# Optimization experiments

Measured on AMD Instinct MI355X. Metric: run time of the kernel, lower is better.

Reference implementation:

```python
import jax, jax.numpy as jnp
import numpy as np

B, N, D, H, KD, VD, O = 64, 2048, 256, 8, 32, 32, 256
LARGE = 1e9
EPS = 1e-10


def setup_inputs() -> dict:
    key = jax.random.key(0)
    ks = jax.random.split(key, 8)
    return {
        "q_data": jax.random.normal(ks[0], (B, N, D), dtype=jnp.float32),
        "m_data": jax.random.normal(ks[1], (B, N, D), dtype=jnp.float32),
        "q_mask": jnp.ones((B, N, 1), dtype=jnp.float32),
        "query_w": jax.random.normal(ks[2], (D, H, KD), dtype=jnp.float32) * 0.05,
        "key_w": jax.random.normal(ks[3], (D, KD), dtype=jnp.float32) * 0.05,
        "value_w": jax.random.normal(ks[4], (D, VD), dtype=jnp.float32) * 0.05,
        "gating_w": jax.random.normal(ks[5], (D, H, VD), dtype=jnp.float32) * 0.05,
        "gating_b": jnp.ones((H, VD), dtype=jnp.float32),
        "output_w": jax.random.normal(ks[6], (H, VD, O), dtype=jnp.float32) * 0.05,
        "output_b": jnp.zeros((O,), dtype=jnp.float32),
    }


def reference(q_data, m_data, q_mask, query_w, key_w, value_w, gating_w, gating_b, output_w, output_b):
    key_dim = query_w.shape[-1]
    # values/keys are shared across heads: [B, N, KD/VD]
    v = jnp.einsum('bka,ac->bkc', m_data, value_w)
    # masked mean over the query axis -> single query per batch element
    q_avg = jnp.sum(q_mask * q_data, axis=1) / (jnp.sum(q_mask, axis=1) + EPS)  # [B, D]
    q = jnp.einsum('ba,ahc->bhc', q_avg, query_w) * (key_dim ** -0.5)  # [B, H, KD]
    k = jnp.einsum('bka,ac->bkc', m_data, key_w)  # [B, N, KD]
    bias = LARGE * (q_mask[:, None, :, 0] - 1.0)  # [B, 1, N]
    logits = jnp.einsum('bhc,bkc->bhk', q, k) + bias  # [B, H, N]
    weights = jax.nn.softmax(logits, axis=-1)
    weighted_avg = jnp.einsum('bhk,bkc->bhc', weights, v)  # [B, H, VD]
    gate = jax.nn.sigmoid(jnp.einsum('bqc,chv->bqhv', q_data, gating_w) + gating_b)  # [B, N, H, VD]
    gated = weighted_avg[:, None] * gate  # broadcast single attn result over queries
    return jnp.einsum('bqhc,hco->bqo', gated, output_w) + output_b  # [B, N, O]
```

## Files before the change

kernel.cpp:

```cpp
#include <hip/hip_runtime.h>

#define B_ 64
#define N_ 2048
#define D_ 256
#define H_ 8
#define LARGE_ 1e9f
#define EPS_ 1e-10f

typedef __attribute__((ext_vector_type(4))) float f32x4;
typedef __attribute__((ext_vector_type(8))) short s16x8;

#define WS_QSUM 0
#define WS_MSUM 65536
#define WS_ZERO 65792
#define WS_QKBF 66048
#define WS_LOG  590336
#define WS_WMP  4784640
#define WS_WGP  6881792
#define WS_WPP  7012864

__device__ __forceinline__ unsigned short f2bf(float f) {
  union { float f; unsigned u; } v; v.f = f;
  unsigned r = v.u + 0x7fffu + ((v.u >> 16) & 1u);
  return (unsigned short)(r >> 16);
}
__device__ __forceinline__ float bf2f(unsigned short s) {
  union { unsigned u; float f; } v; v.u = ((unsigned)s) << 16;
  return v.f;
}

__global__ void kA(const float* __restrict__ q_data, const float* __restrict__ q_mask,
                   const float* __restrict__ gating_w, float* __restrict__ q_sum,
                   float* __restrict__ mask_sum, unsigned short* __restrict__ wgp) {
  int blk = blockIdx.x, t = threadIdx.x;
  if (blk < 512) {
    int b = blk >> 3, n0 = (blk & 7) * 256;
    __shared__ float msk[256];
    __shared__ float mred[4];
    msk[t] = q_mask[b * N_ + n0 + t];
    __syncthreads();
    int w = t >> 6, d4 = t & 63;
    const float* qbase = q_data + ((size_t)(b * N_ + n0)) * D_;
    f32x4 acc = {0.f, 0.f, 0.f, 0.f};
    #pragma unroll 4
    for (int i = 0; i < 64; ++i) {
      int r = i * 4 + w;
      f32x4 v = *(const f32x4*)(qbase + (size_t)r * D_ + d4 * 4);
      float mk = msk[r];
      acc += v * mk;
    }
    float* qs = q_sum + b * D_ + d4 * 4;
    atomicAdd(qs + 0, acc[0]);
    atomicAdd(qs + 1, acc[1]);
    atomicAdd(qs + 2, acc[2]);
    atomicAdd(qs + 3, acc[3]);
    float mv = msk[t];
    for (int off = 32; off; off >>= 1) mv += __shfl_xor(mv, off);
    if ((t & 63) == 0) mred[t >> 6] = mv;
    __syncthreads();
    if (t == 0) atomicAdd(&mask_sum[b], mred[0] + mred[1] + mred[2] + mred[3]);
  } else {
    int base = (blk - 512) * 1024;
    for (int i = 0; i < 4; ++i) {
      int a = base + i * 256 + t;
      int sc = a >> 9, l = (a >> 3) & 63, j = a & 7;
      int s = sc >> 4, c = sc & 15, lh = l >> 4, ll = l & 15;
      int k = s * 32 + lh * 8 + j, n = c * 16 + ll;
      wgp[a] = f2bf(gating_w[k * 256 + n]);
    }
  }
}

__global__ void kB(const float* __restrict__ q_sum, const float* __restrict__ mask_sum,
                   const float* __restrict__ query_w, const float* __restrict__ key_w,
                   unsigned short* __restrict__ qkbf) {
  int b = blockIdx.x, t = threadIdx.x;
  __shared__ float qa[256];
  __shared__ float ql[256];
  float inv = 1.f / (mask_sum[b] + EPS_);
  qa[t] = q_sum[b * 256 + t] * inv;
  __syncthreads();
  float s = 0.f;
  #pragma unroll 4
  for (int a = 0; a < 256; ++a) s += qa[a] * query_w[a * 256 + t];
  ql[t] = s * 0.17677669529663687f;
  __syncthreads();
  float v8[8];
  #pragma unroll
  for (int h = 0; h < 8; ++h) {
    float v = 0.f;
    #pragma unroll
    for (int c = 0; c < 32; ++c) v += key_w[t * 32 + c] * ql[h * 32 + c];
    v8[h] = v;
  }
  int si = t >> 5, lh = (t >> 3) & 3, j = t & 7;
  unsigned short* base = qkbf + ((size_t)(b * 8 + si) * 64) * 8;
  #pragma unroll
  for (int h = 0; h < 8; ++h) {
    base[(lh * 16 + h) * 8 + j] = f2bf(v8[h]);
    base[(lh * 16 + 8 + h) * 8 + j] = 0;
  }
}

__global__ void kC(const float* __restrict__ m_data, const float* __restrict__ q_mask,
                   const unsigned short* __restrict__ qkbf, float* __restrict__ logits) {
  int b = blockIdx.y, n0 = blockIdx.x * 64, t = threadIdx.x;
  __shared__ __align__(16) unsigned char sM[64 * 528];
  {
    int w = t >> 6, d4 = t & 63;
    #pragma unroll
    for (int i = 0; i < 16; ++i) {
      int r = i * 4 + w;
      f32x4 v = *(const f32x4*)(m_data + ((size_t)(b * N_ + n0 + r)) * D_ + d4 * 4);
      uint2 pp;
      pp.x = f2bf(v[0]) | ((unsigned)f2bf(v[1]) << 16);
      pp.y = f2bf(v[2]) | ((unsigned)f2bf(v[3]) << 16);
      *(uint2*)(sM + r * 528 + d4 * 8) = pp;
    }
  }
  __syncthreads();
  int lane = t & 63, w = t >> 6;
  int l15 = lane & 15, lhi = lane >> 4;
  const s16x8* A = (const s16x8*)qkbf + (size_t)b * 512;
  s16x8 areg[8];
  #pragma unroll
  for (int s = 0; s < 8; ++s) areg[s] = A[s * 64 + lane];
  f32x4 acc = {0.f, 0.f, 0.f, 0.f};
  int nrow = w * 16 + l15;
  #pragma unroll
  for (int s = 0; s < 8; ++s) {
    s16x8 bfr = *(const s16x8*)(sM + nrow * 528 + s * 64 + lhi * 16);
    acc = __builtin_amdgcn_mfma_f32_16x16x32_bf16(areg[s], bfr, acc, 0, 0, 0);
  }
  if (lhi < 2) {
    int n = n0 + nrow;
    float bias = LARGE_ * (q_mask[b * N_ + n] - 1.f);
    f32x4 st = acc + bias;
    *(f32x4*)(logits + ((size_t)(b * N_ + n)) * 8 + lhi * 4) = st;
  }
}

__global__ void kS(float* __restrict__ wbuf) {
  int b = blockIdx.x, t = threadIdx.x;
  int lane = t & 63, w = t >> 6;
  __shared__ float sred[4][8];
  __shared__ float Mh[8];
  __shared__ float Sh[8];
  f32x4 lv[16];
  f32x4* base = (f32x4*)(wbuf + (size_t)b * N_ * 8) + t * 16;
  #pragma unroll
  for (int i = 0; i < 16; ++i) lv[i] = base[i];
  float pm[8];
  #pragma unroll
  for (int h = 0; h < 8; ++h) pm[h] = -3.4e38f;
  #pragma unroll
  for (int k = 0; k < 8; ++k)
    #pragma unroll
    for (int hh = 0; hh < 2; ++hh)
      #pragma unroll
      for (int c = 0; c < 4; ++c)
        pm[hh * 4 + c] = fmaxf(pm[hh * 4 + c], lv[k * 2 + hh][c]);
  for (int off = 32; off; off >>= 1)
    #pragma unroll
    for (int h = 0; h < 8; ++h) pm[h] = fmaxf(pm[h], __shfl_xor(pm[h], off));
  if (lane == 0)
    #pragma unroll
    for (int h = 0; h < 8; ++h) sred[w][h] = pm[h];
  __syncthreads();
  if (t < 8) Mh[t] = fmaxf(fmaxf(sred[0][t], sred[1][t]), fmaxf(sred[2][t], sred[3][t]));
  __syncthreads();
  float M[8], ps[8];
  #pragma unroll
  for (int h = 0; h < 8; ++h) { M[h] = Mh[h]; ps[h] = 0.f; }
  #pragma unroll
  for (int k = 0; k < 8; ++k)
    #pragma unroll
    for (int hh = 0; hh < 2; ++hh)
      #pragma unroll
      for (int c = 0; c < 4; ++c) {
        float e = __expf(lv[k * 2 + hh][c] - M[hh * 4 + c]);
        lv[k * 2 + hh][c] = e;
        ps[hh * 4 + c] += e;
      }
  for (int off = 32; off; off >>= 1)
    #pragma unroll
    for (int h = 0; h < 8; ++h) ps[h] += __shfl_xor(ps[h], off);
  if (lane == 0)
    #pragma unroll
    for (int h = 0; h < 8; ++h) sred[w][h] = ps[h];
  __syncthreads();
  if (t < 8) Sh[t] = sred[0][t] + sred[1][t] + sred[2][t] + sred[3][t];
  __syncthreads();
  float rs[8];
  #pragma unroll
  for (int h = 0; h < 8; ++h) rs[h] = 1.f / Sh[h];
  #pragma unroll
  for (int k = 0; k < 8; ++k)
    #pragma unroll
    for (int hh = 0; hh < 2; ++hh)
      #pragma unroll
      for (int c = 0; c < 4; ++c) lv[k * 2 + hh][c] *= rs[hh * 4 + c];
  #pragma unroll
  for (int i = 0; i < 16; ++i) base[i] = lv[i];
}

__global__ void kE(const float* __restrict__ m_data, const float* __restrict__ wbuf,
                   unsigned short* __restrict__ wm_part) {
  int b = blockIdx.y, n0 = blockIdx.x * 256, t = threadIdx.x;
  __shared__ float wb[2048];
  __shared__ float red[4 * 8 * 256];
  {
    const f32x4* src = (const f32x4*)(wbuf + ((size_t)b * N_ + n0) * 8);
    f32x4* dst = (f32x4*)wb;
    dst[t] = src[t];
    dst[t + 256] = src[t + 256];
  }
  __syncthreads();
  int w = t >> 6, l = t & 63;
  f32x4 acc[8];
  #pragma unroll
  for (int h = 0; h < 8; ++h) acc[h] = (f32x4){0.f, 0.f, 0.f, 0.f};
  const float* mbase = m_data + ((size_t)(b * N_ + n0 + w * 64)) * D_ + l * 4;
  #pragma unroll 2
  for (int i = 0; i < 64; ++i) {
    f32x4 mv = *(const f32x4*)(mbase + (size_t)i * D_);
    const f32x4* wrow = (const f32x4*)(wb + (w * 64 + i) * 8);
    f32x4 w0 = wrow[0], w1 = wrow[1];
    acc[0] += mv * w0[0]; acc[1] += mv * w0[1]; acc[2] += mv * w0[2]; acc[3] += mv * w0[3];
    acc[4] += mv * w1[0]; acc[5] += mv * w1[1]; acc[6] += mv * w1[2]; acc[7] += mv * w1[3];
  }
  #pragma unroll
  for (int h = 0; h < 8; ++h) *(f32x4*)(&red[(w * 8 + h) * 256 + l * 4]) = acc[h];
  __syncthreads();
  float s8[8];
  #pragma unroll
  for (int h = 0; h < 8; ++h)
    s8[h] = red[h * 256 + t] + red[(8 + h) * 256 + t] + red[(16 + h) * 256 + t] +
            red[(24 + h) * 256 + t];
  uint4 u;
  u.x = f2bf(s8[0]) | ((unsigned)f2bf(s8[1]) << 16);
  u.y = f2bf(s8[2]) | ((unsigned)f2bf(s8[3]) << 16);
  u.z = f2bf(s8[4]) | ((unsigned)f2bf(s8[5]) << 16);
  u.w = f2bf(s8[6]) | ((unsigned)f2bf(s8[7]) << 16);
  *(uint4*)(wm_part + ((size_t)((b * 8 + blockIdx.x) * 256 + t)) * 8) = u;
}

__global__ void kF(const unsigned short* __restrict__ wm_part, const float* __restrict__ value_w,
                   const float* __restrict__ output_w, unsigned short* __restrict__ wpp) {
  int blk = blockIdx.x, t = threadIdx.x;
  int b = blk >> 2, quad = blk & 3;
  __shared__ float wml[8 * 256];
  __shared__ float wa[256];
  {
    float s8[8] = {0.f, 0.f, 0.f, 0.f, 0.f, 0.f, 0.f, 0.f};
    #pragma unroll
    for (int p = 0; p < 8; ++p) {
      uint4 u = *(const uint4*)(wm_part + ((size_t)((b * 8 + p) * 256 + t)) * 8);
      s8[0] += bf2f(u.x & 0xffff); s8[1] += bf2f(u.x >> 16);
      s8[2] += bf2f(u.y & 0xffff); s8[3] += bf2f(u.y >> 16);
      s8[4] += bf2f(u.z & 0xffff); s8[5] += bf2f(u.z >> 16);
      s8[6] += bf2f(u.w & 0xffff); s8[7] += bf2f(u.w >> 16);
    }
    #pragma unroll
    for (int h = 0; h < 8; ++h) wml[h * 256 + t] = s8[h];
  }
  __syncthreads();
  {
    int h = t >> 5, v = t & 31;
    float s = 0.f;
    #pragma unroll 4
    for (int d = 0; d < 256; ++d) s += wml[h * 256 + d] * value_w[d * 32 + v];
    wa[t] = s;
  }
  __syncthreads();
  unsigned short* wp = wpp + (size_t)b * 65536;
  int base = quad * 16384;
  for (int it = 0; it < 64; ++it) {
    int a = base + it * 256 + t;
    int sc = a >> 9, l = (a >> 3) & 63, j = a & 7;
    int s = sc >> 4, c = sc & 15, lh = l >> 4, ll = l & 15;
    int hv = s * 32 + lh * 8 + j, o = c * 16 + ll;
    wp[a] = f2bf(wa[hv] * output_w[hv * 256 + o]);
  }
}

__global__ void __launch_bounds__(256, 4) kG(
    const float* __restrict__ q_data, const float* __restrict__ gating_b,
    const float* __restrict__ output_b, const unsigned short* __restrict__ wgp,
    const unsigned short* __restrict__ wpp, float* __restrict__ out) {
  int b = blockIdx.y, row0 = blockIdx.x * 64, t = threadIdx.x;
  __shared__ __align__(16) unsigned char sG[64 * 528];
  {
    int w = t >> 6, d4 = t & 63;
    #pragma unroll
    for (int i = 0; i < 16; ++i) {
      int r = i * 4 + w;
      f32x4 v = *(const f32x4*)(q_data + ((size_t)(b * N_ + row0 + r)) * D_ + d4 * 4);
      uint2 pp;
      pp.x = f2bf(v[0]) | ((unsigned)f2bf(v[1]) << 16);
      pp.y = f2bf(v[2]) | ((unsigned)f2bf(v[3]) << 16);
      *(uint2*)(sG + r * 528 + d4 * 8) = pp;
    }
  }
  __syncthreads();
  int lane = t & 63, cg = t >> 6;
  int l15 = lane & 15, lhi = lane >> 4;
  const f32x4 z = {0.f, 0.f, 0.f, 0.f};
  f32x4 acc[16];
  #pragma unroll
  for (int f = 0; f < 16; ++f) acc[f] = z;
  const s16x8* Bg = (const s16x8*)wgp;
  #pragma unroll
  for (int s = 0; s < 8; ++s) {
    s16x8 af[4], bfr[4];
    #pragma unroll
    for (int rt = 0; rt < 4; ++rt)
      af[rt] = *(const s16x8*)(sG + (rt * 16 + l15) * 528 + s * 64 + lhi * 16);
    #pragma unroll
    for (int ct = 0; ct < 4; ++ct) bfr[ct] = Bg[(s * 16 + cg * 4 + ct) * 64 + lane];
    #pragma unroll
    for (int rt = 0; rt < 4; ++rt)
      #pragma unroll
      for (int ct = 0; ct < 4; ++ct)
        acc[rt * 4 + ct] =
            __builtin_amdgcn_mfma_f32_16x16x32_bf16(af[rt], bfr[ct], acc[rt * 4 + ct], 0, 0, 0);
  }
  __syncthreads();
  {
    float gb[4];
    #pragma unroll
    for (int ct = 0; ct < 4; ++ct) gb[ct] = gating_b[cg * 64 + ct * 16 + l15];
    #pragma unroll
    for (int rt = 0; rt < 4; ++rt)
      #pragma unroll
      for (int ct = 0; ct < 4; ++ct) {
        int col = cg * 64 + ct * 16 + l15;
        #pragma unroll
        for (int r = 0; r < 4; ++r) {
          float x = acc[rt * 4 + ct][r] + gb[ct];
          float g = 1.f / (1.f + __expf(-x));
          int row = rt * 16 + lhi * 4 + r;
          *(unsigned short*)(sG + row * 528 + col * 2) = f2bf(g);
        }
      }
  }
  __syncthreads();
  #pragma unroll
  for (int f = 0; f < 16; ++f) acc[f] = z;
  const s16x8* Bp = (const s16x8*)wpp + (size_t)b * 8192;
  #pragma unroll
  for (int s = 0; s < 8; ++s) {
    s16x8 af[4], bfr[4];
    #pragma unroll
    for (int rt = 0; rt < 4; ++rt)
      af[rt] = *(const s16x8*)(sG + (rt * 16 + l15) * 528 + s * 64 + lhi * 16);
    #pragma unroll
    for (int ct = 0; ct < 4; ++ct) bfr[ct] = Bp[(s * 16 + cg * 4 + ct) * 64 + lane];
    #pragma unroll
    for (int rt = 0; rt < 4; ++rt)
      #pragma unroll
      for (int ct = 0; ct < 4; ++ct)
        acc[rt * 4 + ct] =
            __builtin_amdgcn_mfma_f32_16x16x32_bf16(af[rt], bfr[ct], acc[rt * 4 + ct], 0, 0, 0);
  }
  __syncthreads();
  float* fOut = (float*)sG;
  float ob[4];
  #pragma unroll
  for (int ct = 0; ct < 4; ++ct) ob[ct] = output_b[cg * 64 + ct * 16 + l15];
  #pragma unroll
  for (int p = 0; p < 2; ++p) {
    #pragma unroll
    for (int rt2 = 0; rt2 < 2; ++rt2) {
      int rt = p * 2 + rt2;
      #pragma unroll
      for (int ct = 0; ct < 4; ++ct) {
        int col = cg * 64 + ct * 16 + l15;
        #pragma unroll
        for (int r = 0; r < 4; ++r)
          fOut[(rt2 * 16 + lhi * 4 + r) * 260 + col] = acc[rt * 4 + ct][r] + ob[ct];
      }
    }
    __syncthreads();
    {
      int w = t >> 6, c4 = t & 63;
      #pragma unroll
      for (int j = 0; j < 8; ++j) {
        int r32 = j * 4 + w;
        f32x4 v = *(const f32x4*)(fOut + r32 * 260 + c4 * 4);
        *(f32x4*)(out + ((size_t)(b * N_ + row0 + p * 32 + r32)) * D_ + c4 * 4) = v;
      }
    }
    __syncthreads();
  }
}

extern "C" void kernel_launch(void* const* d_in, const int* in_sizes, int n_in,
                              void* d_out, int out_size, void* d_ws, size_t ws_size,
                              hipStream_t stream) {
  const float* q_data   = (const float*)d_in[0];
  const float* m_data   = (const float*)d_in[1];
  const float* q_mask   = (const float*)d_in[2];
  const float* query_w  = (const float*)d_in[3];
  const float* key_w    = (const float*)d_in[4];
  const float* value_w  = (const float*)d_in[5];
  const float* gating_w = (const float*)d_in[6];
  const float* gating_b = (const float*)d_in[7];
  const float* output_w = (const float*)d_in[8];
  const float* output_b = (const float*)d_in[9];
  float* out = (float*)d_out;
  char* ws = (char*)d_ws;

  float* q_sum = (float*)(ws + WS_QSUM);
  float* msum  = (float*)(ws + WS_MSUM);
  unsigned short* qkbf = (unsigned short*)(ws + WS_QKBF);
  float* logits = (float*)(ws + WS_LOG);
  unsigned short* wmp = (unsigned short*)(ws + WS_WMP);
  unsigned short* wgp = (unsigned short*)(ws + WS_WGP);
  unsigned short* wpp = (unsigned short*)(ws + WS_WPP);

  hipMemsetAsync(d_ws, 0, WS_ZERO, stream);
  kA<<<576, 256, 0, stream>>>(q_data, q_mask, gating_w, q_sum, msum, wgp);
  kB<<<64, 256, 0, stream>>>(q_sum, msum, query_w, key_w, qkbf);
  kC<<<dim3(32, 64), 256, 0, stream>>>(m_data, q_mask, qkbf, logits);
  kS<<<64, 256, 0, stream>>>(logits);
  kE<<<dim3(8, 64), 256, 0, stream>>>(m_data, logits, wmp);
  kF<<<256, 256, 0, stream>>>(wmp, value_w, output_w, wpp);
  kG<<<dim3(32, 64), 256, 0, stream>>>(q_data, gating_b, output_b, wgp, wpp, out);
}
```

Measured before the change: 511.8 us.

## Fuse logits, softmax and value accumulation into one online-softmax pass

Merges the logits, softmax and weighted-sum kernels into a single kernel. Each 64-row chunk computes its local max, exp-sum and exp-weighted m_data sum directly from the bf16 tile already staged in shared memory, so m_data is read only once and the logits buffer round trip goes away. A new reduction kernel rescales the 32 per-chunk partials by the global max and divides by the total denominator. The kA atomics and the workspace memset are replaced with per-block partials that kB sums. In exchange, the weighted sum now uses bf16-rounded m_data and the partial buffer is four times larger.

```diff
diff --git a/kernel.cpp b/kernel.cpp
--- a/kernel.cpp
+++ b/kernel.cpp
@@ -10,14 +10,15 @@
 typedef __attribute__((ext_vector_type(4))) float f32x4;
 typedef __attribute__((ext_vector_type(8))) short s16x8;
 
-#define WS_QSUM 0
-#define WS_MSUM 65536
-#define WS_ZERO 65792
-#define WS_QKBF 66048
-#define WS_LOG  590336
-#define WS_WMP  4784640
-#define WS_WGP  6881792
-#define WS_WPP  7012864
+#define WS_QKBF 0
+#define WS_WGP  524288
+#define WS_QPART 655360
+#define WS_MPART 1179648
+#define WS_MX   1181696
+#define WS_SM   1247232
+#define WS_WA   1312768
+#define WS_WMP  1378304
+#define WS_WPP  1378304
 
 __device__ __forceinline__ unsigned short f2bf(float f) {
   union { float f; unsigned u; } v; v.f = f;
@@ -30,12 +31,13 @@
 }
 
 __global__ void kA(const float* __restrict__ q_data, const float* __restrict__ q_mask,
-                   const float* __restrict__ gating_w, float* __restrict__ q_sum,
-                   float* __restrict__ mask_sum, unsigned short* __restrict__ wgp) {
+                   const float* __restrict__ gating_w, float* __restrict__ qpart,
+                   float* __restrict__ mpart, unsigned short* __restrict__ wgp) {
   int blk = blockIdx.x, t = threadIdx.x;
   if (blk < 512) {
     int b = blk >> 3, n0 = (blk & 7) * 256;
     __shared__ float msk[256];
+    __shared__ float qred[4][256];
     __shared__ float mred[4];
     msk[t] = q_mask[b * N_ + n0 + t];
     __syncthreads();
@@ -49,16 +51,13 @@
       float mk = msk[r];
       acc += v * mk;
     }
-    float* qs = q_sum + b * D_ + d4 * 4;
-    atomicAdd(qs + 0, acc[0]);
-    atomicAdd(qs + 1, acc[1]);
-    atomicAdd(qs + 2, acc[2]);
-    atomicAdd(qs + 3, acc[3]);
+    *(f32x4*)(&qred[w][d4 * 4]) = acc;
     float mv = msk[t];
     for (int off = 32; off; off >>= 1) mv += __shfl_xor(mv, off);
     if ((t & 63) == 0) mred[t >> 6] = mv;
     __syncthreads();
-    if (t == 0) atomicAdd(&mask_sum[b], mred[0] + mred[1] + mred[2] + mred[3]);
+    qpart[((size_t)blk) * 256 + t] = qred[0][t] + qred[1][t] + qred[2][t] + qred[3][t];
+    if (t == 0) mpart[blk] = mred[0] + mred[1] + mred[2] + mred[3];
   } else {
     int base = (blk - 512) * 1024;
     for (int i = 0; i < 4; ++i) {
@@ -71,19 +70,24 @@
   }
 }
 
-__global__ void kB(const float* __restrict__ q_sum, const float* __restrict__ mask_sum,
+__global__ void kB(const float* __restrict__ qpart, const float* __restrict__ mpart,
                    const float* __restrict__ query_w, const float* __restrict__ key_w,
                    unsigned short* __restrict__ qkbf) {
   int b = blockIdx.x, t = threadIdx.x;
   __shared__ float qa[256];
   __shared__ float ql[256];
-  float inv = 1.f / (mask_sum[b] + EPS_);
-  qa[t] = q_sum[b * 256 + t] * inv;
-  __syncthreads();
   float s = 0.f;
+  #pragma unroll
+  for (int p = 0; p < 8; ++p) s += qpart[((size_t)(b * 8 + p)) * 256 + t];
+  float ms = 0.f;
+  #pragma unroll
+  for (int p = 0; p < 8; ++p) ms += mpart[b * 8 + p];
+  qa[t] = s / (ms + EPS_);
+  __syncthreads();
+  float acc = 0.f;
   #pragma unroll 4
-  for (int a = 0; a < 256; ++a) s += qa[a] * query_w[a * 256 + t];
-  ql[t] = s * 0.17677669529663687f;
+  for (int a = 0; a < 256; ++a) acc += qa[a] * query_w[a * 256 + t];
+  ql[t] = acc * 0.17677669529663687f;
   __syncthreads();
   float v8[8];
   #pragma unroll
@@ -102,10 +106,14 @@
   }
 }
 
-__global__ void kC(const float* __restrict__ m_data, const float* __restrict__ q_mask,
-                   const unsigned short* __restrict__ qkbf, float* __restrict__ logits) {
-  int b = blockIdx.y, n0 = blockIdx.x * 64, t = threadIdx.x;
+__global__ void kM(const float* __restrict__ m_data, const float* __restrict__ q_mask,
+                   const unsigned short* __restrict__ qkbf, unsigned short* __restrict__ wm_part,
+                   float* __restrict__ mx_part, float* __restrict__ sm_part) {
+  int b = blockIdx.y, ch = blockIdx.x, n0 = ch * 64, t = threadIdx.x;
   __shared__ __align__(16) unsigned char sM[64 * 528];
+  __shared__ f32x4 pW[64][2];
+  __shared__ float red[4][8];
+  __shared__ float hval[8];
   {
     int w = t >> 6, d4 = t & 63;
     #pragma unroll
@@ -132,146 +140,126 @@
     s16x8 bfr = *(const s16x8*)(sM + nrow * 528 + s * 64 + lhi * 16);
     acc = __builtin_amdgcn_mfma_f32_16x16x32_bf16(areg[s], bfr, acc, 0, 0, 0);
   }
+  float bias = LARGE_ * (q_mask[b * N_ + n0 + nrow] - 1.f);
+  float lg[4];
+  #pragma unroll
+  for (int r = 0; r < 4; ++r) lg[r] = (lhi < 2) ? (acc[r] + bias) : -3.4e38f;
+  #pragma unroll
+  for (int off = 8; off; off >>= 1)
+    #pragma unroll
+    for (int r = 0; r < 4; ++r) lg[r] = fmaxf(lg[r], __shfl_xor(lg[r], off));
+  if (l15 == 0 && lhi < 2)
+    #pragma unroll
+    for (int r = 0; r < 4; ++r) red[w][lhi * 4 + r] = lg[r];
+  __syncthreads();
+  if (t < 8) {
+    float m = fmaxf(fmaxf(red[0][t], red[1][t]), fmaxf(red[2][t], red[3][t]));
+    hval[t] = m;
+    mx_part[((size_t)(b * 32 + ch)) * 8 + t] = m;
+  }
+  __syncthreads();
+  float pv[4], ps[4];
+  #pragma unroll
+  for (int r = 0; r < 4; ++r) {
+    float M = hval[(lhi & 1) * 4 + r];
+    float e = __expf(acc[r] + bias - M);
+    pv[r] = e;
+    ps[r] = (lhi < 2) ? e : 0.f;
+  }
   if (lhi < 2) {
-    int n = n0 + nrow;
-    float bias = LARGE_ * (q_mask[b * N_ + n] - 1.f);
-    f32x4 st = acc + bias;
-    *(f32x4*)(logits + ((size_t)(b * N_ + n)) * 8 + lhi * 4) = st;
-  }
-}
-
-__global__ void kS(float* __restrict__ wbuf) {
-  int b = blockIdx.x, t = threadIdx.x;
-  int lane = t & 63, w = t >> 6;
-  __shared__ float sred[4][8];
-  __shared__ float Mh[8];
-  __shared__ float Sh[8];
-  f32x4 lv[16];
-  f32x4* base = (f32x4*)(wbuf + (size_t)b * N_ * 8) + t * 16;
-  #pragma unroll
-  for (int i = 0; i < 16; ++i) lv[i] = base[i];
-  float pm[8];
-  #pragma unroll
-  for (int h = 0; h < 8; ++h) pm[h] = -3.4e38f;
-  #pragma unroll
-  for (int k = 0; k < 8; ++k)
-    #pragma unroll
-    for (int hh = 0; hh < 2; ++hh)
-      #pragma unroll
-      for (int c = 0; c < 4; ++c)
-        pm[hh * 4 + c] = fmaxf(pm[hh * 4 + c], lv[k * 2 + hh][c]);
-  for (int off = 32; off; off >>= 1)
-    #pragma unroll
-    for (int h = 0; h < 8; ++h) pm[h] = fmaxf(pm[h], __shfl_xor(pm[h], off));
-  if (lane == 0)
-    #pragma unroll
-    for (int h = 0; h < 8; ++h) sred[w][h] = pm[h];
-  __syncthreads();
-  if (t < 8) Mh[t] = fmaxf(fmaxf(sred[0][t], sred[1][t]), fmaxf(sred[2][t], sred[3][t]));
-  __syncthreads();
-  float M[8], ps[8];
-  #pragma unroll
-  for (int h = 0; h < 8; ++h) { M[h] = Mh[h]; ps[h] = 0.f; }
-  #pragma unroll
-  for (int k = 0; k < 8; ++k)
-    #pragma unroll
-    for (int hh = 0; hh < 2; ++hh)
-      #pragma unroll
-      for (int c = 0; c < 4; ++c) {
-        float e = __expf(lv[k * 2 + hh][c] - M[hh * 4 + c]);
-        lv[k * 2 + hh][c] = e;
-        ps[hh * 4 + c] += e;
-      }
-  for (int off = 32; off; off >>= 1)
-    #pragma unroll
-    for (int h = 0; h < 8; ++h) ps[h] += __shfl_xor(ps[h], off);
-  if (lane == 0)
-    #pragma unroll
-    for (int h = 0; h < 8; ++h) sred[w][h] = ps[h];
-  __syncthreads();
-  if (t < 8) Sh[t] = sred[0][t] + sred[1][t] + sred[2][t] + sred[3][t];
-  __syncthreads();
-  float rs[8];
-  #pragma unroll
-  for (int h = 0; h < 8; ++h) rs[h] = 1.f / Sh[h];
-  #pragma unroll
-  for (int k = 0; k < 8; ++k)
-    #pragma unroll
-    for (int hh = 0; hh < 2; ++hh)
-      #pragma unroll
-      for (int c = 0; c < 4; ++c) lv[k * 2 + hh][c] *= rs[hh * 4 + c];
-  #pragma unroll
-  for (int i = 0; i < 16; ++i) base[i] = lv[i];
-}
-
-__global__ void kE(const float* __restrict__ m_data, const float* __restrict__ wbuf,
-                   unsigned short* __restrict__ wm_part) {
-  int b = blockIdx.y, n0 = blockIdx.x * 256, t = threadIdx.x;
-  __shared__ float wb[2048];
-  __shared__ float red[4 * 8 * 256];
-  {
-    const f32x4* src = (const f32x4*)(wbuf + ((size_t)b * N_ + n0) * 8);
-    f32x4* dst = (f32x4*)wb;
-    dst[t] = src[t];
-    dst[t + 256] = src[t + 256];
-  }
-  __syncthreads();
-  int w = t >> 6, l = t & 63;
-  f32x4 acc[8];
-  #pragma unroll
-  for (int h = 0; h < 8; ++h) acc[h] = (f32x4){0.f, 0.f, 0.f, 0.f};
-  const float* mbase = m_data + ((size_t)(b * N_ + n0 + w * 64)) * D_ + l * 4;
-  #pragma unroll 2
-  for (int i = 0; i < 64; ++i) {
-    f32x4 mv = *(const f32x4*)(mbase + (size_t)i * D_);
-    const f32x4* wrow = (const f32x4*)(wb + (w * 64 + i) * 8);
-    f32x4 w0 = wrow[0], w1 = wrow[1];
-    acc[0] += mv * w0[0]; acc[1] += mv * w0[1]; acc[2] += mv * w0[2]; acc[3] += mv * w0[3];
-    acc[4] += mv * w1[0]; acc[5] += mv * w1[1]; acc[6] += mv * w1[2]; acc[7] += mv * w1[3];
-  }
-  #pragma unroll
-  for (int h = 0; h < 8; ++h) *(f32x4*)(&red[(w * 8 + h) * 256 + l * 4]) = acc[h];
+    f32x4 pq = {pv[0], pv[1], pv[2], pv[3]};
+    pW[nrow][lhi] = pq;
+  }
+  #pragma unroll
+  for (int off = 8; off; off >>= 1)
+    #pragma unroll
+    for (int r = 0; r < 4; ++r) ps[r] += __shfl_xor(ps[r], off);
+  if (l15 == 0 && lhi < 2)
+    #pragma unroll
+    for (int r = 0; r < 4; ++r) red[w][lhi * 4 + r] = ps[r];
+  __syncthreads();
+  if (t < 8)
+    sm_part[((size_t)(b * 32 + ch)) * 8 + t] = red[0][t] + red[1][t] + red[2][t] + red[3][t];
+  f32x4 vacc[8];
+  #pragma unroll
+  for (int h = 0; h < 8; ++h) vacc[h] = (f32x4){0.f, 0.f, 0.f, 0.f};
+  #pragma unroll 4
+  for (int i = 0; i < 16; ++i) {
+    int r = w * 16 + i;
+    uint2 pp = *(const uint2*)(sM + r * 528 + lane * 8);
+    f32x4 mv;
+    mv[0] = bf2f(pp.x & 0xffff); mv[1] = bf2f(pp.x >> 16);
+    mv[2] = bf2f(pp.y & 0xffff); mv[3] = bf2f(pp.y >> 16);
+    f32x4 w0 = pW[r][0], w1 = pW[r][1];
+    vacc[0] += mv * w0[0]; vacc[1] += mv * w0[1]; vacc[2] += mv * w0[2]; vacc[3] += mv * w0[3];
+    vacc[4] += mv * w1[0]; vacc[5] += mv * w1[1]; vacc[6] += mv * w1[2]; vacc[7] += mv * w1[3];
+  }
+  __syncthreads();
+  float* red2 = (float*)sM;
+  #pragma unroll
+  for (int h = 0; h < 8; ++h) *(f32x4*)(&red2[(w * 8 + h) * 256 + lane * 4]) = vacc[h];
   __syncthreads();
   float s8[8];
   #pragma unroll
   for (int h = 0; h < 8; ++h)
-    s8[h] = red[h * 256 + t] + red[(8 + h) * 256 + t] + red[(16 + h) * 256 + t] +
-            red[(24 + h) * 256 + t];
+    s8[h] = red2[h * 256 + t] + red2[(8 + h) * 256 + t] + red2[(16 + h) * 256 + t] +
+            red2[(24 + h) * 256 + t];
   uint4 u;
   u.x = f2bf(s8[0]) | ((unsigned)f2bf(s8[1]) << 16);
   u.y = f2bf(s8[2]) | ((unsigned)f2bf(s8[3]) << 16);
   u.z = f2bf(s8[4]) | ((unsigned)f2bf(s8[5]) << 16);
   u.w = f2bf(s8[6]) | ((unsigned)f2bf(s8[7]) << 16);
-  *(uint4*)(wm_part + ((size_t)((b * 8 + blockIdx.x) * 256 + t)) * 8) = u;
-}
-
-__global__ void kF(const unsigned short* __restrict__ wm_part, const float* __restrict__ value_w,
-                   const float* __restrict__ output_w, unsigned short* __restrict__ wpp) {
+  *(uint4*)(wm_part + ((size_t)((b * 32 + ch) * 256 + t)) * 8) = u;
+}
+
+__global__ void kF1(const unsigned short* __restrict__ wm_part, const float* __restrict__ mx_part,
+                    const float* __restrict__ sm_part, const float* __restrict__ value_w,
+                    float* __restrict__ wa_g) {
+  int b = blockIdx.x, t = threadIdx.x;
+  __shared__ float s_mx[256], s_sm[256], scl[256];
+  __shared__ float gmx[8], gden[8];
+  __shared__ float wml[8][256];
+  s_mx[t] = mx_part[(size_t)b * 256 + t];
+  s_sm[t] = sm_part[(size_t)b * 256 + t];
+  __syncthreads();
+  if (t < 8) {
+    float m = -3.4e38f;
+    for (int c = 0; c < 32; ++c) m = fmaxf(m, s_mx[c * 8 + t]);
+    gmx[t] = m;
+  }
+  __syncthreads();
+  scl[t] = __expf(s_mx[t] - gmx[t & 7]);
+  __syncthreads();
+  if (t < 8) {
+    float d = 0.f;
+    for (int c = 0; c < 32; ++c) d += s_sm[c * 8 + t] * scl[c * 8 + t];
+    gden[t] = d;
+  }
+  float acc[8] = {0.f, 0.f, 0.f, 0.f, 0.f, 0.f, 0.f, 0.f};
+  for (int c = 0; c < 32; ++c) {
+    uint4 u = *(const uint4*)(wm_part + ((size_t)((b * 32 + c) * 256 + t)) * 8);
+    const float* sc = &scl[c * 8];
+    acc[0] += bf2f(u.x & 0xffff) * sc[0]; acc[1] += bf2f(u.x >> 16) * sc[1];
+    acc[2] += bf2f(u.y & 0xffff) * sc[2]; acc[3] += bf2f(u.y >> 16) * sc[3];
+    acc[4] += bf2f(u.z & 0xffff) * sc[4]; acc[5] += bf2f(u.z >> 16) * sc[5];
+    acc[6] += bf2f(u.w & 0xffff) * sc[6]; acc[7] += bf2f(u.w >> 16) * sc[7];
+  }
+  #pragma unroll
+  for (int h = 0; h < 8; ++h) wml[h][t] = acc[h];
+  __syncthreads();
+  int h = t >> 5, v = t & 31;
+  float s = 0.f;
+  #pragma unroll 4
+  for (int d = 0; d < 256; ++d) s += wml[h][d] * value_w[d * 32 + v];
+  wa_g[b * 256 + t] = s / gden[h];
+}
+
+__global__ void kF2(const float* __restrict__ wa_g, const float* __restrict__ output_w,
+                    unsigned short* __restrict__ wpp) {
   int blk = blockIdx.x, t = threadIdx.x;
   int b = blk >> 2, quad = blk & 3;
-  __shared__ float wml[8 * 256];
   __shared__ float wa[256];
-  {
-    float s8[8] = {0.f, 0.f, 0.f, 0.f, 0.f, 0.f, 0.f, 0.f};
-    #pragma unroll
-    for (int p = 0; p < 8; ++p) {
-      uint4 u = *(const uint4*)(wm_part + ((size_t)((b * 8 + p) * 256 + t)) * 8);
-      s8[0] += bf2f(u.x & 0xffff); s8[1] += bf2f(u.x >> 16);
-      s8[2] += bf2f(u.y & 0xffff); s8[3] += bf2f(u.y >> 16);
-      s8[4] += bf2f(u.z & 0xffff); s8[5] += bf2f(u.z >> 16);
-      s8[6] += bf2f(u.w & 0xffff); s8[7] += bf2f(u.w >> 16);
-    }
-    #pragma unroll
-    for (int h = 0; h < 8; ++h) wml[h * 256 + t] = s8[h];
-  }
-  __syncthreads();
-  {
-    int h = t >> 5, v = t & 31;
-    float s = 0.f;
-    #pragma unroll 4
-    for (int d = 0; d < 256; ++d) s += wml[h * 256 + d] * value_w[d * 32 + v];
-    wa[t] = s;
-  }
+  wa[t] = wa_g[b * 256 + t];
   __syncthreads();
   unsigned short* wp = wpp + (size_t)b * 65536;
   int base = quad * 16384;
@@ -411,20 +399,20 @@
   float* out = (float*)d_out;
   char* ws = (char*)d_ws;
 
-  float* q_sum = (float*)(ws + WS_QSUM);
-  float* msum  = (float*)(ws + WS_MSUM);
   unsigned short* qkbf = (unsigned short*)(ws + WS_QKBF);
-  float* logits = (float*)(ws + WS_LOG);
+  unsigned short* wgp  = (unsigned short*)(ws + WS_WGP);
+  float* qpart = (float*)(ws + WS_QPART);
+  float* mpart = (float*)(ws + WS_MPART);
+  float* mx    = (float*)(ws + WS_MX);
+  float* sm    = (float*)(ws + WS_SM);
+  float* wa    = (float*)(ws + WS_WA);
   unsigned short* wmp = (unsigned short*)(ws + WS_WMP);
-  unsigned short* wgp = (unsigned short*)(ws + WS_WGP);
   unsigned short* wpp = (unsigned short*)(ws + WS_WPP);
 
-  hipMemsetAsync(d_ws, 0, WS_ZERO, stream);
-  kA<<<576, 256, 0, stream>>>(q_data, q_mask, gating_w, q_sum, msum, wgp);
-  kB<<<64, 256, 0, stream>>>(q_sum, msum, query_w, key_w, qkbf);
-  kC<<<dim3(32, 64), 256, 0, stream>>>(m_data, q_mask, qkbf, logits);
-  kS<<<64, 256, 0, stream>>>(logits);
-  kE<<<dim3(8, 64), 256, 0, stream>>>(m_data, logits, wmp);
-  kF<<<256, 256, 0, stream>>>(wmp, value_w, output_w, wpp);
+  kA<<<576, 256, 0, stream>>>(q_data, q_mask, gating_w, qpart, mpart, wgp);
+  kB<<<64, 256, 0, stream>>>(qpart, mpart, query_w, key_w, qkbf);
+  kM<<<dim3(32, 64), 256, 0, stream>>>(m_data, q_mask, qkbf, wmp, mx, sm);
+  kF1<<<64, 256, 0, stream>>>(wmp, mx, sm, value_w, wa);
+  kF2<<<256, 256, 0, stream>>>(wa, output_w, wpp);
   kG<<<dim3(32, 64), 256, 0, stream>>>(q_data, gating_b, output_b, wgp, wpp, out);
 }
```

After: 478.4 us. 6.5% less time.
